# Kernel tuning notes

Hardware: AMD Instinct MI355X
Metric: run time of the kernel (lower is better)

The kernel has to match this reference:

```python
import jax, jax.numpy as jnp
import numpy as np

B, T, I, H = 4096, 512, 32, 32


def setup_inputs() -> dict:
    key = jax.random.key(0)
    k = jax.random.split(key, 7)
    s = 1.0 / np.sqrt(H)  # torch uniform(-1/sqrt(H), 1/sqrt(H)) init scale
    x = jax.random.normal(k[0], (B, T, I), dtype=jnp.float32)
    W_ih = jax.random.uniform(k[1], (3 * H, I), minval=-s, maxval=s, dtype=jnp.float32)
    W_hh = jax.random.uniform(k[2], (3 * H, H), minval=-s, maxval=s, dtype=jnp.float32)
    b_ih = jax.random.uniform(k[3], (3 * H,), minval=-s, maxval=s, dtype=jnp.float32)
    b_hh = jax.random.uniform(k[4], (3 * H,), minval=-s, maxval=s, dtype=jnp.float32)
    w_head = jax.random.uniform(k[5], (H,), minval=-s, maxval=s, dtype=jnp.float32)
    b_head = jax.random.uniform(k[6], (1,), minval=-s, maxval=s, dtype=jnp.float32)
    return {"x": x, "W_ih": W_ih, "W_hh": W_hh, "b_ih": b_ih,
            "b_hh": b_hh, "w_head": w_head, "b_head": b_head}


def reference(x, W_ih, W_hh, b_ih, b_hh, w_head, b_head):
    # PyTorch GRU gate order in stacked weights: [reset, update, new]
    h_dim = W_hh.shape[1]
    # Precompute input contribution for all timesteps: [B, T, 3H]
    gx_all = jnp.einsum('bti,gi->btg', x, W_ih) + b_ih

    def step(h, gx):  # h: [B,H], gx: [B,3H]
        gh = h @ W_hh.T + b_hh  # [B,3H]
        r = jax.nn.sigmoid(gx[:, :h_dim] + gh[:, :h_dim])
        z = jax.nn.sigmoid(gx[:, h_dim:2 * h_dim] + gh[:, h_dim:2 * h_dim])
        n = jnp.tanh(gx[:, 2 * h_dim:] + r * gh[:, 2 * h_dim:])
        h_new = (1.0 - z) * n + z * h
        return h_new, None

    h0 = jnp.zeros((x.shape[0], h_dim), dtype=x.dtype)
    last, _ = jax.lax.scan(step, h0, jnp.swapaxes(gx_all, 0, 1))  # scan over T
    # head: Linear(H, 1) then squeeze(-1) -> [B]
    y = last @ w_head + b_head[0]
    return y
```

## Files before the change

kernel.cpp:

```cpp
#include <hip/hip_runtime.h>


#define TSTEPS 512

__global__ __launch_bounds__(256, 2)
void gru_fused_kernel(const float* __restrict__ x,
                      const float* __restrict__ W_ih,
                      const float* __restrict__ W_hh,
                      const float* __restrict__ b_ih,
                      const float* __restrict__ b_hh,
                      const float* __restrict__ w_head,
                      const float* __restrict__ b_head,
                      float* __restrict__ y)
{
    const int tid = threadIdx.x;
    const int hw  = tid >> 5;
    const int j   = tid & 31;
    const int b   = blockIdx.x * 8 + hw;

    __shared__ float sh[8 * 64];
    float* xs = &sh[hw * 64];
    float* hs = xs + 32;

    float wr[32], wz[32], wn[32], ur[32], uz[32], un[32];
#pragma unroll
    for (int k = 0; k < 32; ++k) {
        wr[k] = W_ih[(j)      * 32 + k];
        wz[k] = W_ih[(32 + j) * 32 + k];
        wn[k] = W_ih[(64 + j) * 32 + k];
        ur[k] = W_hh[(j)      * 32 + k];
        uz[k] = W_hh[(32 + j) * 32 + k];
        un[k] = W_hh[(64 + j) * 32 + k];
    }
    const float br  = b_ih[j]      + b_hh[j];
    const float bz  = b_ih[32 + j] + b_hh[32 + j];
    const float bni = b_ih[64 + j];
    const float bnh = b_hh[64 + j];

    float h = 0.0f;
    const float* xp = x + ((size_t)b * TSTEPS) * 32 + j;

    for (int t = 0; t < TSTEPS; ++t) {
        const float xv = xp[(size_t)t * 32];
        xs[j] = xv;
        hs[j] = h;

        float ar = br, az = bz, an = bni, ah = bnh;
        const float4* x4 = (const float4*)xs;
        const float4* h4 = (const float4*)hs;
#pragma unroll
        for (int q = 0; q < 8; ++q) {
            const float4 xq = x4[q];
            const float4 hq = h4[q];
            ar = fmaf(wr[4*q+0], xq.x, ar); ar = fmaf(wr[4*q+1], xq.y, ar);
            ar = fmaf(wr[4*q+2], xq.z, ar); ar = fmaf(wr[4*q+3], xq.w, ar);
            az = fmaf(wz[4*q+0], xq.x, az); az = fmaf(wz[4*q+1], xq.y, az);
            az = fmaf(wz[4*q+2], xq.z, az); az = fmaf(wz[4*q+3], xq.w, az);
            an = fmaf(wn[4*q+0], xq.x, an); an = fmaf(wn[4*q+1], xq.y, an);
            an = fmaf(wn[4*q+2], xq.z, an); an = fmaf(wn[4*q+3], xq.w, an);
            ar = fmaf(ur[4*q+0], hq.x, ar); ar = fmaf(ur[4*q+1], hq.y, ar);
            ar = fmaf(ur[4*q+2], hq.z, ar); ar = fmaf(ur[4*q+3], hq.w, ar);
            az = fmaf(uz[4*q+0], hq.x, az); az = fmaf(uz[4*q+1], hq.y, az);
            az = fmaf(uz[4*q+2], hq.z, az); az = fmaf(uz[4*q+3], hq.w, az);
            ah = fmaf(un[4*q+0], hq.x, ah); ah = fmaf(un[4*q+1], hq.y, ah);
            ah = fmaf(un[4*q+2], hq.z, ah); ah = fmaf(un[4*q+3], hq.w, ah);
        }

        const float r  = 1.0f / (1.0f + __expf(-ar));
        const float z  = 1.0f / (1.0f + __expf(-az));
        const float nv = an + r * ah;
        const float e  = __expf(2.0f * nv);
        const float n  = 1.0f - 2.0f / (e + 1.0f);
        h = n + z * (h - n);
    }

    float acc = h * w_head[j];
#pragma unroll
    for (int m = 16; m >= 1; m >>= 1)
        acc += __shfl_xor(acc, m, 32);
    if (j == 0)
        y[b] = acc + b_head[0];
}

extern "C" void kernel_launch(void* const* d_in, const int* in_sizes, int n_in,
                              void* d_out, int out_size, void* d_ws, size_t ws_size,
                              hipStream_t stream) {
    const float* x      = (const float*)d_in[0];
    const float* W_ih   = (const float*)d_in[1];
    const float* W_hh   = (const float*)d_in[2];
    const float* b_ih   = (const float*)d_in[3];
    const float* b_hh   = (const float*)d_in[4];
    const float* w_head = (const float*)d_in[5];
    const float* b_head = (const float*)d_in[6];
    float* y = (float*)d_out;

    const int B = 4096;
    dim3 grid(B / 8), block(256);
    gru_fused_kernel<<<grid, block, 0, stream>>>(x, W_ih, W_hh, b_ih, b_hh,
                                                 w_head, b_head, y);
}
```

Before: 807.5 us.

## Split GRU reduction across wave halves to halve registers and raise occupancy

Each batch row now uses a full 64-lane wave. The two 32-lane halves each cover half of the K dimension, and their partial gate sums are combined with a cross-half shuffle. This halves the per-thread weight register arrays, which allows launch bounds of 4 blocks per SU and doubles the total number of threads. It also prefetches the next timestep's x value during the current step to hide global load latency. The cost is four extra cross-lane shuffles per step, and each batch row now occupies twice as many lanes.

```diff
diff --git a/kernel.cpp b/kernel.cpp
--- a/kernel.cpp
+++ b/kernel.cpp
@@ -3,7 +3,7 @@
 
 #define TSTEPS 512
 
-__global__ __launch_bounds__(256, 2)
+__global__ __launch_bounds__(256, 4)
 void gru_fused_kernel(const float* __restrict__ x,
                       const float* __restrict__ W_ih,
                       const float* __restrict__ W_hh,
@@ -13,51 +13,56 @@
                       const float* __restrict__ b_head,
                       float* __restrict__ y)
 {
-    const int tid = threadIdx.x;
-    const int hw  = tid >> 5;
-    const int j   = tid & 31;
-    const int b   = blockIdx.x * 8 + hw;
+    const int tid  = threadIdx.x;
+    const int wave = tid >> 6;
+    const int l    = tid & 63;
+    const int j    = l & 31;
+    const int p    = l >> 5;
+    const int b    = blockIdx.x * 4 + wave;
+    const int k0   = p * 16;
 
-    __shared__ float sh[8 * 64];
-    float* xs = &sh[hw * 64];
-    float* hs = xs + 32;
+    __shared__ float sh[4][64];
+    float* s = sh[wave];
 
-    float wr[32], wz[32], wn[32], ur[32], uz[32], un[32];
+    float wr[16], wz[16], wn[16], ur[16], uz[16], un[16];
 #pragma unroll
-    for (int k = 0; k < 32; ++k) {
-        wr[k] = W_ih[(j)      * 32 + k];
-        wz[k] = W_ih[(32 + j) * 32 + k];
-        wn[k] = W_ih[(64 + j) * 32 + k];
-        ur[k] = W_hh[(j)      * 32 + k];
-        uz[k] = W_hh[(32 + j) * 32 + k];
-        un[k] = W_hh[(64 + j) * 32 + k];
+    for (int kk = 0; kk < 16; ++kk) {
+        wr[kk] = W_ih[(j)      * 32 + k0 + kk];
+        wz[kk] = W_ih[(32 + j) * 32 + k0 + kk];
+        wn[kk] = W_ih[(64 + j) * 32 + k0 + kk];
+        ur[kk] = W_hh[(j)      * 32 + k0 + kk];
+        uz[kk] = W_hh[(32 + j) * 32 + k0 + kk];
+        un[kk] = W_hh[(64 + j) * 32 + k0 + kk];
     }
-    const float br  = b_ih[j]      + b_hh[j];
-    const float bz  = b_ih[32 + j] + b_hh[32 + j];
-    const float bni = b_ih[64 + j];
-    const float bnh = b_hh[64 + j];
+    const float br  = p ? 0.0f : (b_ih[j]      + b_hh[j]);
+    const float bz  = p ? 0.0f : (b_ih[32 + j] + b_hh[32 + j]);
+    const float bni = p ? 0.0f : b_ih[64 + j];
+    const float bnh = p ? 0.0f : b_hh[64 + j];
 
-    float h = 0.0f;
-    const float* xp = x + ((size_t)b * TSTEPS) * 32 + j;
+    const float* xrow = x + (size_t)b * TSTEPS * 32;
 
+    float h  = 0.0f;
+    float xv = xrow[j];
+
+    #pragma unroll 1
     for (int t = 0; t < TSTEPS; ++t) {
-        const float xv = xp[(size_t)t * 32];
-        xs[j] = xv;
-        hs[j] = h;
+        s[l] = (l < 32) ? xv : h;
+
+        const int tn = (t + 1 < TSTEPS) ? (t + 1) : t;
+        xv = xrow[(size_t)tn * 32 + j];
 
         float ar = br, az = bz, an = bni, ah = bnh;
-        const float4* x4 = (const float4*)xs;
-        const float4* h4 = (const float4*)hs;
+        const float4* S4 = (const float4*)s;
 #pragma unroll
-        for (int q = 0; q < 8; ++q) {
-            const float4 xq = x4[q];
-            const float4 hq = h4[q];
+        for (int q = 0; q < 4; ++q) {
+            const float4 xq = S4[4 * p + q];
             ar = fmaf(wr[4*q+0], xq.x, ar); ar = fmaf(wr[4*q+1], xq.y, ar);
             ar = fmaf(wr[4*q+2], xq.z, ar); ar = fmaf(wr[4*q+3], xq.w, ar);
             az = fmaf(wz[4*q+0], xq.x, az); az = fmaf(wz[4*q+1], xq.y, az);
             az = fmaf(wz[4*q+2], xq.z, az); az = fmaf(wz[4*q+3], xq.w, az);
             an = fmaf(wn[4*q+0], xq.x, an); an = fmaf(wn[4*q+1], xq.y, an);
             an = fmaf(wn[4*q+2], xq.z, an); an = fmaf(wn[4*q+3], xq.w, an);
+            const float4 hq = S4[8 + 4 * p + q];
             ar = fmaf(ur[4*q+0], hq.x, ar); ar = fmaf(ur[4*q+1], hq.y, ar);
             ar = fmaf(ur[4*q+2], hq.z, ar); ar = fmaf(ur[4*q+3], hq.w, ar);
             az = fmaf(uz[4*q+0], hq.x, az); az = fmaf(uz[4*q+1], hq.y, az);
@@ -65,6 +70,11 @@
             ah = fmaf(un[4*q+0], hq.x, ah); ah = fmaf(un[4*q+1], hq.y, ah);
             ah = fmaf(un[4*q+2], hq.z, ah); ah = fmaf(un[4*q+3], hq.w, ah);
         }
+
+        ar += __shfl_xor(ar, 32);
+        az += __shfl_xor(az, 32);
+        an += __shfl_xor(an, 32);
+        ah += __shfl_xor(ah, 32);
 
         const float r  = 1.0f / (1.0f + __expf(-ar));
         const float z  = 1.0f / (1.0f + __expf(-az));
@@ -77,8 +87,8 @@
     float acc = h * w_head[j];
 #pragma unroll
     for (int m = 16; m >= 1; m >>= 1)
-        acc += __shfl_xor(acc, m, 32);
-    if (j == 0)
+        acc += __shfl_xor(acc, m);
+    if (l == 0)
         y[b] = acc + b_head[0];
 }
 
@@ -95,7 +105,7 @@
     float* y = (float*)d_out;
 
     const int B = 4096;
-    dim3 grid(B / 8), block(256);
+    dim3 grid(B / 4), block(256);
     gru_fused_kernel<<<grid, block, 0, stream>>>(x, W_ih, W_hh, b_ih, b_hh,
                                                  w_head, b_head, y);
 }
```

Result: slower. 948.3 us (+17.4%).
